# Optimization experiments

Hardware: AMD Instinct MI355X
Metric: run time of the kernel (lower is better)

## Reference

```python
import jax, jax.numpy as jnp
import numpy as np

B, Cin, H, W = 8, 256, 32, 32
KS, NH, K = 32, 8, 5          # key_size == value_size, num_heads, kernel_size
STRIDE, PAD = 1, 2
Cout = KS * 3 * NH            # 768
EPS = 1e-5


def setup_inputs() -> dict:
    key = jax.random.key(0)
    k0, k1, k2 = jax.random.split(key, 3)
    return {
        "x": jax.random.normal(k0, (B, Cin, H, W), jnp.float32),
        "conv_w": jax.random.normal(k1, (Cout, Cin), jnp.float32) / np.sqrt(Cin).astype(np.float32),
        "conv_b": jax.random.normal(k2, (Cout,), jnp.float32) * 0.02,
        "gn_w": jnp.ones((Cout,), jnp.float32),
        "gn_b": jnp.zeros((Cout,), jnp.float32),
    }


def reference(x, conv_w, conv_b, gn_w, gn_b):
    Bb = x.shape[0]
    OH = (H + 2 * PAD - K) // STRIDE + 1
    OW = (W + 2 * PAD - K) // STRIDE + 1

    # 1x1 conv: (B, Cout, H, W)
    attn = jnp.einsum('bchw,oc->bohw', x, conv_w) + conv_b[None, :, None, None]

    # unfold / Tile2d -> (B, KH, KW, Cout, OH, OW)
    ap = jnp.pad(attn, ((0, 0), (0, 0), (PAD, PAD), (PAD, PAD)))
    rows = []
    for kh in range(K):
        cols = [ap[:, :, kh:kh + OH * STRIDE:STRIDE, kw:kw + OW * STRIDE:STRIDE]
                for kw in range(K)]
        rows.append(jnp.stack(cols, axis=1))          # (B, KW, C, OH, OW)
    tiles = jnp.stack(rows, axis=1)                   # (B, KH, KW, C, OH, OW)

    # GroupNorm over (group_channels, OH, OW) per (b, kh, kw) sample.
    # groups = 3*NH, group size = KS (each head's key/query/value chunk).
    G = 3 * NH
    t = tiles.reshape(Bb, K, K, G, KS, OH, OW)
    mean = t.mean(axis=(4, 5, 6), keepdims=True)
    var = t.var(axis=(4, 5, 6), keepdims=True)        # biased, like torch GroupNorm
    t = (t - mean) * jax.lax.rsqrt(var + EPS)
    t = t.reshape(Bb, K, K, Cout, OH, OW)
    t = t * gn_w[None, None, None, :, None, None] + gn_b[None, None, None, :, None, None]

    # (B, OH, OW, NH, 3*KS, KH*KW)
    t = t.transpose(0, 4, 5, 3, 1, 2).reshape(Bb, OH, OW, NH, 3 * KS, K * K)
    keyt = t[..., :KS, :]            # (B, OH, OW, NH, KS, KK)
    qt = t[..., KS:2 * KS, :]
    vt = t[..., 2 * KS:, :]          # (B, OH, OW, NH, VS, KK)

    q = qt.mean(axis=-1)             # mean query over the window: (B, OH, OW, NH, KS)
    sal = jnp.einsum('bijnk,bijnkp->bijnp', q, keyt) / np.float32(np.sqrt(KS))
    mask = jax.nn.softmax(sal, axis=-1)               # (B, OH, OW, NH, KK)
    out = jnp.einsum('bijnvp,bijnp->bijnv', vt, mask)  # (B, OH, OW, NH, VS)

    out = out.transpose(0, 3, 4, 1, 2).reshape(Bb, NH * KS, OH, OW)
    return out
```

## Files before the change

### kernel.cpp

```cpp
#include <hip/hip_runtime.h>
#include <hip/hip_bf16.h>

#define B_    8
#define CIN   256
#define COUT  768
#define G_    24
#define PW    40
#define PLANE 1440
#define EPS_  1e-5f

typedef float f32x4 __attribute__((ext_vector_type(4)));
typedef short s16x8 __attribute__((ext_vector_type(8)));
typedef unsigned short ushort_t;
typedef unsigned short u16x4 __attribute__((ext_vector_type(4)));
typedef unsigned long long ull_t;

#define LDS_FENCE() do { asm volatile("" ::: "memory"); \
                         __builtin_amdgcn_s_waitcnt(0xC07F); \
                         asm volatile("" ::: "memory"); } while (0)

static __device__ __forceinline__ ushort_t f2bf(float f) {
    union { float f; unsigned u; } a; a.f = f;
    const unsigned u = a.u;
    const unsigned r = u + 0x7FFFu + ((u >> 16) & 1u);
    return (ushort_t)(r >> 16);
}
static __device__ __forceinline__ float bf2f(ushort_t h) {
    union { unsigned u; float f; } a; a.u = ((unsigned)h) << 16; return a.f;
}
static __device__ __forceinline__ void st4(float* dst, u16x4 v) {
    *(f32x4*)dst = f32x4{ bf2f(v[0]), bf2f(v[1]), bf2f(v[2]), bf2f(v[3]) };
}
static __device__ __forceinline__ unsigned pk2(float lo, float hi) {
    return (unsigned)f2bf(lo) | ((unsigned)f2bf(hi) << 16);
}

__launch_bounds__(256)
__global__ void conv_gemm(const float* __restrict__ wsrc, const float* __restrict__ x,
                          const float* __restrict__ bias, ushort_t* __restrict__ attn,
                          float* __restrict__ rowAgg) {
    const int t = threadIdx.x;
    const int wv = t >> 6, lane = t & 63;
    const int q = lane >> 4, l15 = lane & 15;
    const int m0 = blockIdx.y * 64;
    const int mw = wv * 16;
    const int n_t = blockIdx.x * 64;
    const int b = n_t >> 10, nl0 = n_t & 1023;
    const int y0 = nl0 >> 5;

    __shared__ ushort_t Bs[64][264];
    ushort_t (*Ct)[2][44] = (ushort_t (*)[2][44])(&Bs[0][0]);
    float (*red)[11]      = (float (*)[11])((char*)(&Bs[0][0]) + 64 * 2 * 44 * 2);

    {
        const int half = t >> 7;
        const int kp = t & 127;
        const int k2 = kp * 2;
        const float* xr0 = x + (size_t)b * (CIN * 1024) + (size_t)k2 * 1024 + nl0 + half * 32;
        const float* xr1 = xr0 + 1024;
        #pragma unroll
        for (int c = 0; c < 8; ++c) {
            const float4 u0 = *(const float4*)(xr0 + c * 4);
            const float4 u1 = *(const float4*)(xr1 + c * 4);
            const int nn = half * 32 + c * 4;
            *(unsigned*)&Bs[nn + 0][k2] = pk2(u0.x, u1.x);
            *(unsigned*)&Bs[nn + 1][k2] = pk2(u0.y, u1.y);
            *(unsigned*)&Bs[nn + 2][k2] = pk2(u0.z, u1.z);
            *(unsigned*)&Bs[nn + 3][k2] = pk2(u0.w, u1.w);
        }
    }
    __syncthreads();

    const float* aPf = wsrc + (size_t)(m0 + mw + l15) * 256 + q * 8;

    f32x4 acc[4] = {{0,0,0,0},{0,0,0,0},{0,0,0,0},{0,0,0,0}};
    #pragma unroll
    for (int k0 = 0; k0 < 256; k0 += 32) {
        const float4 af0 = *(const float4*)(aPf + k0);
        const float4 af1 = *(const float4*)(aPf + k0 + 4);
        s16x8 a;
        a[0] = (short)f2bf(af0.x); a[1] = (short)f2bf(af0.y);
        a[2] = (short)f2bf(af0.z); a[3] = (short)f2bf(af0.w);
        a[4] = (short)f2bf(af1.x); a[5] = (short)f2bf(af1.y);
        a[6] = (short)f2bf(af1.z); a[7] = (short)f2bf(af1.w);
        const int kk = k0 + q * 8;
        const s16x8 b0 = *(const s16x8*)&Bs[l15 +  0][kk];
        const s16x8 b1 = *(const s16x8*)&Bs[l15 + 16][kk];
        const s16x8 b2 = *(const s16x8*)&Bs[l15 + 32][kk];
        const s16x8 b3 = *(const s16x8*)&Bs[l15 + 48][kk];
        acc[0] = __builtin_amdgcn_mfma_f32_16x16x32_bf16(a, b0, acc[0], 0, 0, 0);
        acc[1] = __builtin_amdgcn_mfma_f32_16x16x32_bf16(a, b1, acc[1], 0, 0, 0);
        acc[2] = __builtin_amdgcn_mfma_f32_16x16x32_bf16(a, b2, acc[2], 0, 0, 0);
        acc[3] = __builtin_amdgcn_mfma_f32_16x16x32_bf16(a, b3, acc[3], 0, 0, 0);
    }
    __syncthreads();

    float bb[4];
    #pragma unroll
    for (int r = 0; r < 4; ++r) bb[r] = bias[m0 + mw + q * 4 + r];
    #pragma unroll
    for (int j = 0; j < 4; ++j) {
        const int yy = j >> 1, xx = (j & 1) * 16 + l15;
        #pragma unroll
        for (int r = 0; r < 4; ++r)
            Ct[mw + q * 4 + r][yy][2 + xx] = f2bf(acc[j][r] + bb[r]);
    }
    #pragma unroll
    for (int it = 0; it < 2; ++it) {
        const int id = it * 256 + t;
        const int m = id >> 3, yy = (id >> 2) & 1, pos = id & 3;
        const int us = (pos == 0) ? 0 : (32 + 2 * pos);
        *(unsigned*)&Ct[m][yy][us] = 0u;
    }
    __syncthreads();

    ushort_t* pb = attn + ((size_t)(b * COUT + m0)) * PLANE;
    #pragma unroll
    for (int it = 0; it < 5; ++it) {
        const int id = it * 256 + t;
        const int m = id / 20, rem = id % 20, yy = rem / 10, s = rem % 10;
        const ull_t v = *(const ull_t*)&Ct[m][yy][s * 4];
        *(ull_t*)(pb + (size_t)m * PLANE + (y0 + yy + 2) * PW + s * 4) = v;
    }
    if (y0 == 0 || y0 == 30) {
        const int rowA = (y0 == 0) ? 0 : 34;
        #pragma unroll
        for (int it = 0; it < 5; ++it) {
            const int id = it * 256 + t;
            const int m = id / 20, rem = id % 20, yy = rem / 10, s = rem % 10;
            *(ull_t*)(pb + (size_t)m * PLANE + (rowA + yy) * PW + s * 4) = 0ull;
        }
    }

    if (t < 128) {
        const int gi = t >> 6, yy = (t >> 5) & 1, c = t & 31;
        const int m = gi * 32 + c;
        float lin = 0.f, sq = 0.f, e0 = 0.f, e1 = 0.f, e30 = 0.f, e31 = 0.f;
        #pragma unroll
        for (int u = 0; u < 9; ++u) {
            const ull_t vv = *(const ull_t*)&Ct[m][yy][u * 4];
            const unsigned lo = (unsigned)vv, hi = (unsigned)(vv >> 32);
            union { unsigned u; float f; } f0, f1, f2, f3;
            f0.u = lo << 16; f1.u = lo & 0xffff0000u;
            f2.u = hi << 16; f3.u = hi & 0xffff0000u;
            lin += (f0.f + f1.f) + (f2.f + f3.f);
            sq  += (f0.f * f0.f + f1.f * f1.f) + (f2.f * f2.f + f3.f * f3.f);
            if (u == 0) { e0 = f2.f; e1 = f3.f; }
            if (u == 8) { e30 = f0.f; e31 = f1.f; }
        }
        red[t][0] = lin; red[t][1] = sq;
        red[t][2] = e0;  red[t][3] = e0 * e0;
        red[t][4] = e1;  red[t][5] = e1 * e1;
        red[t][6] = e30; red[t][7] = e30 * e30;
        red[t][8] = e31; red[t][9] = e31 * e31;
    }
    __syncthreads();
    if (t < 40) {
        const int s = t % 10, gy = t / 10;
        const int gi = gy >> 1, yy = gy & 1;
        float sum = 0.f;
        #pragma unroll
        for (int c = 0; c < 32; ++c) sum += red[gi * 64 + yy * 32 + c][s];
        const int g = blockIdx.y * 2 + gi;
        rowAgg[(((size_t)b * G_ + g) * 32 + (y0 + yy)) * 10 + s] = sum;
    }
}

__launch_bounds__(64)
__global__ void local_attn(const ushort_t* __restrict__ attn,
                           const float* __restrict__ rowAgg,
                           const float* __restrict__ gn_w, const float* __restrict__ gn_b,
                           float* __restrict__ out) {
    const int wid = blockIdx.x;
    const int b = wid >> 8;
    const int n = (wid >> 5) & 7;
    const int i0 = wid & 31;
    const int t = threadIdx.x;
    const int h = t >> 5;
    const int j = t & 31;

    __shared__ float KB[2][2][208];
    __shared__ float QB[2][2][208];
    __shared__ float rpL[96][5], rp2L[96][5];
    __shared__ float s_m[75], s_r[75];
    __shared__ float s_rq[25], s_mq[25], s_rk[25], s_ck[25], s_rv[25], s_cv[25];
    __shared__ float s_gw[96], s_gb[96];

    s_gw[t] = gn_w[n * 96 + t];
    s_gb[t] = gn_b[n * 96 + t];
    if (t < 32) {
        s_gw[64 + t] = gn_w[n * 96 + 64 + t];
        s_gb[64 + t] = gn_b[n * 96 + 64 + t];
    }

    const float* rab = rowAgg + (size_t)((b * G_ + n * 3) * 32) * 10;
    #pragma unroll
    for (int pass = 0; pass < 2; ++pass) {
        const int e = (pass == 0) ? t : 64 + t;
        if (pass == 0 || t < 32) {
            const float* a = rab + (size_t)e * 10;
            const float S = a[0], Sq = a[1];
            const float e0 = a[2], q0 = a[3], e1 = a[4], q1 = a[5];
            const float e30 = a[6], q30 = a[7], e31 = a[8], q31 = a[9];
            rpL[e][0] = S - e30 - e31; rpL[e][1] = S - e31; rpL[e][2] = S;
            rpL[e][3] = S - e0;        rpL[e][4] = S - e0 - e1;
            rp2L[e][0] = Sq - q30 - q31; rp2L[e][1] = Sq - q31; rp2L[e][2] = Sq;
            rp2L[e][3] = Sq - q0;        rp2L[e][4] = Sq - q0 - q1;
        }
    }
    __syncthreads();

    #pragma unroll
    for (int pass = 0; pass < 2; ++pass) {
        const int e = (pass == 0) ? t : 64 + t;
        if (e < 75) {
            const int gi = e / 25, p = e % 25;
            const int kw = p % 5, kh = p / 5;
            const int rb = gi * 32;
            float cs = 0.f, cs2 = 0.f;
            #pragma unroll
            for (int yy = 0; yy < 32; ++yy) { cs += rpL[rb + yy][kw]; cs2 += rp2L[rb + yy][kw]; }
            if (kh == 0)      { cs -= rpL[rb + 30][kw] + rpL[rb + 31][kw]; cs2 -= rp2L[rb + 30][kw] + rp2L[rb + 31][kw]; }
            else if (kh == 1) { cs -= rpL[rb + 31][kw];                    cs2 -= rp2L[rb + 31][kw]; }
            else if (kh == 3) { cs -= rpL[rb + 0][kw];                     cs2 -= rp2L[rb + 0][kw]; }
            else if (kh == 4) { cs -= rpL[rb + 0][kw] + rpL[rb + 1][kw];   cs2 -= rp2L[rb + 0][kw] + rp2L[rb + 1][kw]; }
            const float inv_n = 1.f / 32768.f;
            const float mean = cs * inv_n;
            const float var  = cs2 * inv_n - mean * mean;
            s_m[e] = mean;
            s_r[e] = rsqrtf(var + EPS_);
        }
    }
    __syncthreads();

    if (t < 25) {
        const float mK = s_m[t],      rK = s_r[t];
        const float mQ = s_m[25 + t], rQ = s_r[25 + t];
        const float mV = s_m[50 + t], rV = s_r[50 + t];
        s_rk[t] = rK; s_ck[t] = mK * rK;
        s_rq[t] = rQ; s_mq[t] = mQ * rQ;
        s_rv[t] = rV; s_cv[t] = mV * rV;
    }
    __syncthreads();

    float rq[25]; float cQ = 0.f;
    #pragma unroll
    for (int p = 0; p < 25; ++p) { rq[p] = s_rq[p]; cQ += s_mq[p]; }

    const ushort_t* regB = attn + (size_t)(b * COUT + n * 96) * PLANE + i0 * PW;
    const bool stg = (j < 25);
    const int eo1 = j * 4, eo2 = (j + 25) * 4;

    const ushort_t* baseK = regB + (size_t)(h * 16) * PLANE;
    const ushort_t* baseQ = regB + (size_t)(32 + h * 16) * PLANE;
    const ushort_t* baseV = regB + (size_t)(64 + h * 16) * PLANE;

    u16x4 nK1{0,0,0,0}, nK2{0,0,0,0}, nQ1{0,0,0,0}, nQ2{0,0,0,0};
    u16x4 fK1{0,0,0,0}, fK2{0,0,0,0}, fQ1{0,0,0,0}, fQ2{0,0,0,0};
    if (stg) {
        const u16x4 a1 = *(const u16x4*)(baseK + eo1), a2 = *(const u16x4*)(baseK + eo2);
        const u16x4 q1 = *(const u16x4*)(baseQ + eo1), q2 = *(const u16x4*)(baseQ + eo2);
        st4(&KB[h][0][eo1], a1); st4(&KB[h][0][eo2], a2);
        st4(&QB[h][0][eo1], q1); st4(&QB[h][0][eo2], q2);
        nK1 = *(const u16x4*)(baseK + PLANE + eo1); nK2 = *(const u16x4*)(baseK + PLANE + eo2);
        nQ1 = *(const u16x4*)(baseQ + PLANE + eo1); nQ2 = *(const u16x4*)(baseQ + PLANE + eo2);
        fK1 = *(const u16x4*)(baseK + 2 * (size_t)PLANE + eo1);
        fK2 = *(const u16x4*)(baseK + 2 * (size_t)PLANE + eo2);
        fQ1 = *(const u16x4*)(baseQ + 2 * (size_t)PLANE + eo1);
        fQ2 = *(const u16x4*)(baseQ + 2 * (size_t)PLANE + eo2);
    }
    LDS_FENCE();

    float sal[25];
    #pragma unroll
    for (int p = 0; p < 25; ++p) sal[p] = 0.f;
    float sumQ2 = 0.f, sumQB = 0.f;

    for (int cc = 0; cc < 16; ++cc) {
        const int buf = cc & 1;
        if (stg && cc < 15) {
            st4(&KB[h][buf ^ 1][eo1], nK1); st4(&KB[h][buf ^ 1][eo2], nK2);
            st4(&QB[h][buf ^ 1][eo1], nQ1); st4(&QB[h][buf ^ 1][eo2], nQ2);
            nK1 = fK1; nK2 = fK2; nQ1 = fQ1; nQ2 = fQ2;
            if (cc < 13) {
                fK1 = *(const u16x4*)(baseK + (size_t)(cc + 3) * PLANE + eo1);
                fK2 = *(const u16x4*)(baseK + (size_t)(cc + 3) * PLANE + eo2);
                fQ1 = *(const u16x4*)(baseQ + (size_t)(cc + 3) * PLANE + eo1);
                fQ2 = *(const u16x4*)(baseQ + (size_t)(cc + 3) * PLANE + eo2);
            } else if (cc == 13) {
                fK1 = *(const u16x4*)(baseV + eo1);
                fK2 = *(const u16x4*)(baseV + eo2);
                fQ1 = *(const u16x4*)(baseV + (size_t)PLANE + eo1);
                fQ2 = *(const u16x4*)(baseV + (size_t)PLANE + eo2);
            }
        }
        const int ch = h * 16 + cc;
        const float* qb = &QB[h][buf][j];
        const float* kb = &KB[h][buf][j];
        float qa0 = 0.f, qa1 = 0.f, qa2 = 0.f, qa3 = 0.f, qa4 = 0.f;
        #pragma unroll
        for (int kw = 0; kw < 5; ++kw) {
            qa0 += rq[0 * 5 + kw] * qb[0 * PW + kw];
            qa1 += rq[1 * 5 + kw] * qb[1 * PW + kw];
            qa2 += rq[2 * 5 + kw] * qb[2 * PW + kw];
            qa3 += rq[3 * 5 + kw] * qb[3 * PW + kw];
            qa4 += rq[4 * 5 + kw] * qb[4 * PW + kw];
        }
        const float qa = (qa0 + qa1) + (qa2 + qa3) + qa4;
        const float qk  = s_gw[32 + ch] * ((qa - cQ) * 0.04f) + s_gb[32 + ch];
        const float qk2 = qk * s_gw[ch];
        sumQ2 += qk2; sumQB += qk * s_gb[ch];
        #pragma unroll
        for (int kh = 0; kh < 5; ++kh)
            #pragma unroll
            for (int kw = 0; kw < 5; ++kw)
                sal[kh * 5 + kw] += qk2 * kb[kh * PW + kw];
        LDS_FENCE();
    }

    u16x4 vA1 = nQ1, vA2 = nQ2, vB1{0,0,0,0}, vB2{0,0,0,0};
    if (stg) {
        st4(&KB[h][0][eo1], nK1); st4(&KB[h][0][eo2], nK2);
        vB1 = *(const u16x4*)(baseV + 2 * (size_t)PLANE + eo1);
        vB2 = *(const u16x4*)(baseV + 2 * (size_t)PLANE + eo2);
    }

    sumQ2 += __shfl_xor(sumQ2, 32);
    sumQB += __shfl_xor(sumQB, 32);
    #pragma unroll
    for (int p = 0; p < 25; ++p) sal[p] += __shfl_xor(sal[p], 32);

    #pragma unroll
    for (int p = 0; p < 25; ++p) sal[p] = s_rk[p] * sal[p] - s_ck[p] * sumQ2 + sumQB;

    const float scale = 0.17677669529663687f;
    float mmax = -3.4e38f;
    #pragma unroll
    for (int p = 0; p < 25; ++p) { sal[p] *= scale; mmax = fmaxf(mmax, sal[p]); }
    float ssum = 0.f;
    #pragma unroll
    for (int p = 0; p < 25; ++p) { sal[p] = __expf(sal[p] - mmax); ssum += sal[p]; }
    const float rs = 1.f / ssum;
    float cV2 = 0.f;
    #pragma unroll
    for (int p = 0; p < 25; ++p) {
        const float m = sal[p] * rs;
        sal[p] = m * s_rv[p];
        cV2 += m * s_cv[p];
    }
    LDS_FENCE();

    for (int cc = 0; cc < 16; ++cc) {
        const int buf = cc & 1;
        if (stg && cc < 15) {
            st4(&KB[h][buf ^ 1][eo1], vA1); st4(&KB[h][buf ^ 1][eo2], vA2);
            vA1 = vB1; vA2 = vB2;
            if (cc < 13) {
                vB1 = *(const u16x4*)(baseV + (size_t)(cc + 3) * PLANE + eo1);
                vB2 = *(const u16x4*)(baseV + (size_t)(cc + 3) * PLANE + eo2);
            }
        }
        const int v = h * 16 + cc;
        const float* vb = &KB[h][buf][j];
        float a0 = 0.f, a1 = 0.f, a2 = 0.f, a3 = 0.f, a4 = 0.f;
        #pragma unroll
        for (int kw = 0; kw < 5; ++kw) {
            a0 += sal[0 * 5 + kw] * vb[0 * PW + kw];
            a1 += sal[1 * 5 + kw] * vb[1 * PW + kw];
            a2 += sal[2 * 5 + kw] * vb[2 * PW + kw];
            a3 += sal[3 * 5 + kw] * vb[3 * PW + kw];
            a4 += sal[4 * 5 + kw] * vb[4 * PW + kw];
        }
        const float acc = (a0 + a1) + (a2 + a3) + a4;
        out[((size_t)(b * 256 + n * 32 + v) * 32 + i0) * 32 + j] =
            s_gw[64 + v] * acc + (s_gb[64 + v] - s_gw[64 + v] * cV2);
        LDS_FENCE();
    }
}

extern "C" void kernel_launch(void* const* d_in, const int* in_sizes, int n_in,
                              void* d_out, int out_size, void* d_ws, size_t ws_size,
                              hipStream_t stream) {
    const float* x      = (const float*)d_in[0];
    const float* conv_w = (const float*)d_in[1];
    const float* conv_b = (const float*)d_in[2];
    const float* gn_w   = (const float*)d_in[3];
    const float* gn_b   = (const float*)d_in[4];
    float* out = (float*)d_out;

    ushort_t* attn    = (ushort_t*)d_ws;
    float*    rowAgg  = (float*)(attn + 8847360);

    conv_gemm<<<dim3(128, 12), 256, 0, stream>>>(conv_w, x, conv_b, attn, rowAgg);
    local_attn<<<2048, 64, 0, stream>>>(attn, rowAgg, gn_w, gn_b, out);
}
```

Baseline: 123.8 us.

## Process two output rows per block in local_attn with 128-thread blocks

Each local_attn block now covers two adjacent output rows. It uses two 64-lane waves, each handling half the channels, and each wave covers both rows (32 lanes per row). The staged 6-row window (240 floats) is shared by both rows, so redundant bf16 loads and the per-block GroupNorm statistics setup are amortised over twice the output. The cross-half reduction of saliencies now goes through an LDS exchange buffer and a __syncthreads instead of a wave shuffle. The trade-offs are fewer blocks, more LDS per block, and a block-level barrier.

```diff
diff --git a/kernel.cpp b/kernel.cpp
--- a/kernel.cpp
+++ b/kernel.cpp
@@ -166,70 +166,60 @@
     }
 }
 
-__launch_bounds__(64)
+__launch_bounds__(128)
 __global__ void local_attn(const ushort_t* __restrict__ attn,
                            const float* __restrict__ rowAgg,
                            const float* __restrict__ gn_w, const float* __restrict__ gn_b,
                            float* __restrict__ out) {
     const int wid = blockIdx.x;
-    const int b = wid >> 8;
-    const int n = (wid >> 5) & 7;
-    const int i0 = wid & 31;
+    const int b = wid >> 7;
+    const int n = (wid >> 4) & 7;
+    const int i0 = (wid & 15) * 2;
     const int t = threadIdx.x;
-    const int h = t >> 5;
-    const int j = t & 31;
-
-    __shared__ float KB[2][2][208];
-    __shared__ float QB[2][2][208];
+    const int h = t >> 6;
+    const int lane = t & 63;
+    const int r = lane >> 5;
+    const int j = lane & 31;
+
+    __shared__ float KB[2][2][240];
+    __shared__ float QB[2][2][240];
+    __shared__ float ex[128][27];
     __shared__ float rpL[96][5], rp2L[96][5];
     __shared__ float s_m[75], s_r[75];
     __shared__ float s_rq[25], s_mq[25], s_rk[25], s_ck[25], s_rv[25], s_cv[25];
     __shared__ float s_gw[96], s_gb[96];
 
-    s_gw[t] = gn_w[n * 96 + t];
-    s_gb[t] = gn_b[n * 96 + t];
-    if (t < 32) {
-        s_gw[64 + t] = gn_w[n * 96 + 64 + t];
-        s_gb[64 + t] = gn_b[n * 96 + 64 + t];
-    }
+    if (t < 96) { s_gw[t] = gn_w[n * 96 + t]; s_gb[t] = gn_b[n * 96 + t]; }
 
     const float* rab = rowAgg + (size_t)((b * G_ + n * 3) * 32) * 10;
-    #pragma unroll
-    for (int pass = 0; pass < 2; ++pass) {
-        const int e = (pass == 0) ? t : 64 + t;
-        if (pass == 0 || t < 32) {
-            const float* a = rab + (size_t)e * 10;
-            const float S = a[0], Sq = a[1];
-            const float e0 = a[2], q0 = a[3], e1 = a[4], q1 = a[5];
-            const float e30 = a[6], q30 = a[7], e31 = a[8], q31 = a[9];
-            rpL[e][0] = S - e30 - e31; rpL[e][1] = S - e31; rpL[e][2] = S;
-            rpL[e][3] = S - e0;        rpL[e][4] = S - e0 - e1;
-            rp2L[e][0] = Sq - q30 - q31; rp2L[e][1] = Sq - q31; rp2L[e][2] = Sq;
-            rp2L[e][3] = Sq - q0;        rp2L[e][4] = Sq - q0 - q1;
-        }
-    }
-    __syncthreads();
-
-    #pragma unroll
-    for (int pass = 0; pass < 2; ++pass) {
-        const int e = (pass == 0) ? t : 64 + t;
-        if (e < 75) {
-            const int gi = e / 25, p = e % 25;
-            const int kw = p % 5, kh = p / 5;
-            const int rb = gi * 32;
-            float cs = 0.f, cs2 = 0.f;
-            #pragma unroll
-            for (int yy = 0; yy < 32; ++yy) { cs += rpL[rb + yy][kw]; cs2 += rp2L[rb + yy][kw]; }
-            if (kh == 0)      { cs -= rpL[rb + 30][kw] + rpL[rb + 31][kw]; cs2 -= rp2L[rb + 30][kw] + rp2L[rb + 31][kw]; }
-            else if (kh == 1) { cs -= rpL[rb + 31][kw];                    cs2 -= rp2L[rb + 31][kw]; }
-            else if (kh == 3) { cs -= rpL[rb + 0][kw];                     cs2 -= rp2L[rb + 0][kw]; }
-            else if (kh == 4) { cs -= rpL[rb + 0][kw] + rpL[rb + 1][kw];   cs2 -= rp2L[rb + 0][kw] + rp2L[rb + 1][kw]; }
-            const float inv_n = 1.f / 32768.f;
-            const float mean = cs * inv_n;
-            const float var  = cs2 * inv_n - mean * mean;
-            s_m[e] = mean;
-            s_r[e] = rsqrtf(var + EPS_);
-        }
+    if (t < 96) {
+        const float* a = rab + (size_t)t * 10;
+        const float S = a[0], Sq = a[1];
+        const float e0 = a[2], q0 = a[3], e1 = a[4], q1 = a[5];
+        const float e30 = a[6], q30 = a[7], e31 = a[8], q31 = a[9];
+        rpL[t][0] = S - e30 - e31; rpL[t][1] = S - e31; rpL[t][2] = S;
+        rpL[t][3] = S - e0;        rpL[t][4] = S - e0 - e1;
+        rp2L[t][0] = Sq - q30 - q31; rp2L[t][1] = Sq - q31; rp2L[t][2] = Sq;
+        rp2L[t][3] = Sq - q0;        rp2L[t][4] = Sq - q0 - q1;
+    }
+    __syncthreads();
+
+    if (t < 75) {
+        const int gi = t / 25, p = t % 25;
+        const int kw = p % 5, kh = p / 5;
+        const int rb = gi * 32;
+        float cs = 0.f, cs2 = 0.f;
+        #pragma unroll
+        for (int yy = 0; yy < 32; ++yy) { cs += rpL[rb + yy][kw]; cs2 += rp2L[rb + yy][kw]; }
+        if (kh == 0)      { cs -= rpL[rb + 30][kw] + rpL[rb + 31][kw]; cs2 -= rp2L[rb + 30][kw] + rp2L[rb + 31][kw]; }
+        else if (kh == 1) { cs -= rpL[rb + 31][kw];                    cs2 -= rp2L[rb + 31][kw]; }
+        else if (kh == 3) { cs -= rpL[rb + 0][kw];                     cs2 -= rp2L[rb + 0][kw]; }
+        else if (kh == 4) { cs -= rpL[rb + 0][kw] + rpL[rb + 1][kw];   cs2 -= rp2L[rb + 0][kw] + rp2L[rb + 1][kw]; }
+        const float inv_n = 1.f / 32768.f;
+        const float mean = cs * inv_n;
+        const float var  = cs2 * inv_n - mean * mean;
+        s_m[t] = mean;
+        s_r[t] = rsqrtf(var + EPS_);
     }
     __syncthreads();
 
@@ -248,26 +238,24 @@
     for (int p = 0; p < 25; ++p) { rq[p] = s_rq[p]; cQ += s_mq[p]; }
 
     const ushort_t* regB = attn + (size_t)(b * COUT + n * 96) * PLANE + i0 * PW;
-    const bool stg = (j < 25);
-    const int eo1 = j * 4, eo2 = (j + 25) * 4;
+    const bool stg = (lane < 60);
+    const int eo = lane * 4;
+    const int base = r * PW + j;
 
     const ushort_t* baseK = regB + (size_t)(h * 16) * PLANE;
     const ushort_t* baseQ = regB + (size_t)(32 + h * 16) * PLANE;
     const ushort_t* baseV = regB + (size_t)(64 + h * 16) * PLANE;
 
-    u16x4 nK1{0,0,0,0}, nK2{0,0,0,0}, nQ1{0,0,0,0}, nQ2{0,0,0,0};
-    u16x4 fK1{0,0,0,0}, fK2{0,0,0,0}, fQ1{0,0,0,0}, fQ2{0,0,0,0};
+    u16x4 nK{0,0,0,0}, nQ{0,0,0,0}, fK{0,0,0,0}, fQ{0,0,0,0};
     if (stg) {
-        const u16x4 a1 = *(const u16x4*)(baseK + eo1), a2 = *(const u16x4*)(baseK + eo2);
-        const u16x4 q1 = *(const u16x4*)(baseQ + eo1), q2 = *(const u16x4*)(baseQ + eo2);
-        st4(&KB[h][0][eo1], a1); st4(&KB[h][0][eo2], a2);
-        st4(&QB[h][0][eo1], q1); st4(&QB[h][0][eo2], q2);
-        nK1 = *(const u16x4*)(baseK + PLANE + eo1); nK2 = *(const u16x4*)(baseK + PLANE + eo2);
-        nQ1 = *(const u16x4*)(baseQ + PLANE + eo1); nQ2 = *(const u16x4*)(baseQ + PLANE + eo2);
-        fK1 = *(const u16x4*)(baseK + 2 * (size_t)PLANE + eo1);
-        fK2 = *(const u16x4*)(baseK + 2 * (size_t)PLANE + eo2);
-        fQ1 = *(const u16x4*)(baseQ + 2 * (size_t)PLANE + eo1);
-        fQ2 = *(const u16x4*)(baseQ + 2 * (size_t)PLANE + eo2);
+        const u16x4 c0K = *(const u16x4*)(baseK + eo);
+        const u16x4 c0Q = *(const u16x4*)(baseQ + eo);
+        st4(&KB[h][0][eo], c0K);
+        st4(&QB[h][0][eo], c0Q);
+        nK = *(const u16x4*)(baseK + (size_t)PLANE + eo);
+        nQ = *(const u16x4*)(baseQ + (size_t)PLANE + eo);
+        fK = *(const u16x4*)(baseK + 2 * (size_t)PLANE + eo);
+        fQ = *(const u16x4*)(baseQ + 2 * (size_t)PLANE + eo);
     }
     LDS_FENCE();
 
@@ -279,24 +267,20 @@
     for (int cc = 0; cc < 16; ++cc) {
         const int buf = cc & 1;
         if (stg && cc < 15) {
-            st4(&KB[h][buf ^ 1][eo1], nK1); st4(&KB[h][buf ^ 1][eo2], nK2);
-            st4(&QB[h][buf ^ 1][eo1], nQ1); st4(&QB[h][buf ^ 1][eo2], nQ2);
-            nK1 = fK1; nK2 = fK2; nQ1 = fQ1; nQ2 = fQ2;
+            st4(&KB[h][buf ^ 1][eo], nK);
+            st4(&QB[h][buf ^ 1][eo], nQ);
+            nK = fK; nQ = fQ;
             if (cc < 13) {
-                fK1 = *(const u16x4*)(baseK + (size_t)(cc + 3) * PLANE + eo1);
-                fK2 = *(const u16x4*)(baseK + (size_t)(cc + 3) * PLANE + eo2);
-                fQ1 = *(const u16x4*)(baseQ + (size_t)(cc + 3) * PLANE + eo1);
-                fQ2 = *(const u16x4*)(baseQ + (size_t)(cc + 3) * PLANE + eo2);
+                fK = *(const u16x4*)(baseK + (size_t)(cc + 3) * PLANE + eo);
+                fQ = *(const u16x4*)(baseQ + (size_t)(cc + 3) * PLANE + eo);
             } else if (cc == 13) {
-                fK1 = *(const u16x4*)(baseV + eo1);
-                fK2 = *(const u16x4*)(baseV + eo2);
-                fQ1 = *(const u16x4*)(baseV + (size_t)PLANE + eo1);
-                fQ2 = *(const u16x4*)(baseV + (size_t)PLANE + eo2);
+                fK = *(const u16x4*)(baseV + eo);
+                fQ = *(const u16x4*)(baseV + (size_t)PLANE + eo);
             }
         }
         const int ch = h * 16 + cc;
-        const float* qb = &QB[h][buf][j];
-        const float* kb = &KB[h][buf][j];
+        const float* qb = &QB[h][buf][base];
+        const float* kb = &KB[h][buf][base];
         float qa0 = 0.f, qa1 = 0.f, qa2 = 0.f, qa3 = 0.f, qa4 = 0.f;
         #pragma unroll
         for (int kw = 0; kw < 5; ++kw) {
@@ -318,17 +302,18 @@
         LDS_FENCE();
     }
 
-    u16x4 vA1 = nQ1, vA2 = nQ2, vB1{0,0,0,0}, vB2{0,0,0,0};
-    if (stg) {
-        st4(&KB[h][0][eo1], nK1); st4(&KB[h][0][eo2], nK2);
-        vB1 = *(const u16x4*)(baseV + 2 * (size_t)PLANE + eo1);
-        vB2 = *(const u16x4*)(baseV + 2 * (size_t)PLANE + eo2);
-    }
-
-    sumQ2 += __shfl_xor(sumQ2, 32);
-    sumQB += __shfl_xor(sumQB, 32);
-    #pragma unroll
-    for (int p = 0; p < 25; ++p) sal[p] += __shfl_xor(sal[p], 32);
+    #pragma unroll
+    for (int p = 0; p < 25; ++p) ex[t][p] = sal[p];
+    ex[t][25] = sumQ2; ex[t][26] = sumQB;
+    if (stg) st4(&KB[h][0][eo], nK);
+    __syncthreads();
+    const int par = t ^ 64;
+    #pragma unroll
+    for (int p = 0; p < 25; ++p) sal[p] += ex[par][p];
+    sumQ2 += ex[par][25]; sumQB += ex[par][26];
+
+    u16x4 vA = nQ, vB{0,0,0,0};
+    if (stg) vB = *(const u16x4*)(baseV + 2 * (size_t)PLANE + eo);
 
     #pragma unroll
     for (int p = 0; p < 25; ++p) sal[p] = s_rk[p] * sal[p] - s_ck[p] * sumQ2 + sumQB;
@@ -353,15 +338,12 @@
     for (int cc = 0; cc < 16; ++cc) {
         const int buf = cc & 1;
         if (stg && cc < 15) {
-            st4(&KB[h][buf ^ 1][eo1], vA1); st4(&KB[h][buf ^ 1][eo2], vA2);
-            vA1 = vB1; vA2 = vB2;
-            if (cc < 13) {
-                vB1 = *(const u16x4*)(baseV + (size_t)(cc + 3) * PLANE + eo1);
-                vB2 = *(const u16x4*)(baseV + (size_t)(cc + 3) * PLANE + eo2);
-            }
+            st4(&KB[h][buf ^ 1][eo], vA);
+            vA = vB;
+            if (cc < 13) vB = *(const u16x4*)(baseV + (size_t)(cc + 3) * PLANE + eo);
         }
         const int v = h * 16 + cc;
-        const float* vb = &KB[h][buf][j];
+        const float* vb = &KB[h][buf][base];
         float a0 = 0.f, a1 = 0.f, a2 = 0.f, a3 = 0.f, a4 = 0.f;
         #pragma unroll
         for (int kw = 0; kw < 5; ++kw) {
@@ -372,7 +354,7 @@
             a4 += sal[4 * 5 + kw] * vb[4 * PW + kw];
         }
         const float acc = (a0 + a1) + (a2 + a3) + a4;
-        out[((size_t)(b * 256 + n * 32 + v) * 32 + i0) * 32 + j] =
+        out[((size_t)(b * 256 + n * 32 + v) * 32 + (i0 + r)) * 32 + j] =
             s_gw[64 + v] * acc + (s_gb[64 + v] - s_gw[64 + v] * cV2);
         LDS_FENCE();
     }
@@ -392,5 +374,5 @@
     float*    rowAgg  = (float*)(attn + 8847360);
 
     conv_gemm<<<dim3(128, 12), 256, 0, stream>>>(conv_w, x, conv_b, attn, rowAgg);
-    local_attn<<<2048, 64, 0, stream>>>(attn, rowAgg, gn_w, gn_b, out);
-}
+    local_attn<<<1024, 128, 0, stream>>>(attn, rowAgg, gn_w, gn_b, out);
+}
```

Result: faster. 119.2 us (-3.8%).
